# Kernel tuning notes

Measured on AMD Instinct MI355X. Metric: run time of the kernel, lower is better.

Reference implementation:

```python
import jax, jax.numpy as jnp
import numpy as np

EPS = 1e-6

def _rmsnorm(x, w):
    # Qwen3RMSNorm over last dim, computed in fp32
    var = jnp.mean(jnp.square(x), axis=-1, keepdims=True)
    return x * jax.lax.rsqrt(var + EPS) * w

def setup_inputs() -> dict:
    key = jax.random.key(0)
    ks = jax.random.split(key, 8)
    NSEQ, IN_DIM, H, G, D, SINK = 16384, 4096, 8, 4, 16, 16
    s = 0.02
    return {
        "hidden_states": jax.random.normal(ks[0], (1, NSEQ, IN_DIM), jnp.float32),
        "q_w": jax.random.normal(ks[1], (H * G * D, IN_DIM), jnp.float32) * s,
        "q_b": jax.random.normal(ks[2], (H * G * D,), jnp.float32) * s,
        "k_w": jax.random.normal(ks[3], (H * D, IN_DIM), jnp.float32) * s,
        "q_norm_w": jnp.ones((D,), jnp.float32),
        "k_norm_w": jnp.ones((D,), jnp.float32),
        "k_base": jax.random.normal(ks[4], (H, 1, SINK, D), jnp.float32) * s,
        "b": jax.random.normal(ks[5], (H, 1, G), jnp.float32) * s,
    }

def reference(hidden_states, q_w, q_b, k_w, q_norm_w, k_norm_w, k_base, b):
    H, _, SINK, D = k_base.shape
    G = b.shape[-1]
    d = jnp.sqrt(jnp.asarray(D, hidden_states.dtype))
    h = hidden_states[0]                                   # [n, in_dim]
    n = h.shape[0]
    # projections + RMSNorm
    q = _rmsnorm((h @ q_w.T + q_b).reshape(n, H, G, D), q_norm_w)   # [n,H,G,D]
    k = _rmsnorm((h @ k_w.T).reshape(n, H, D), k_norm_w)            # [n,H,D]
    # logit: per-token key against its own group queries + learned bias
    logit = jnp.einsum('nhd,nhgd->hng', k, q) / d + b               # [H,n,G]
    # logit_base: learned sink keys against queries
    logit_base = jnp.einsum('hsd,nhgd->hnsg', k_base[:, 0], q) / d  # [H,n,S,G]
    # sigmoid-difference gate, summed over sink tokens
    denom = 1.0 + jnp.sum(jnp.exp(logit_base - logit[:, :, None, :]), axis=2)  # [H,n,G]
    score = jnp.mean(1.0 / denom, axis=-1)                          # [H,n]
    return score[None]                                              # [1,H,n]
```

## Files before the change

kernel.cpp:

```cpp
#include <hip/hip_runtime.h>
#include <hip/hip_bf16.h>

typedef __attribute__((ext_vector_type(8))) short bf16x8;
typedef __attribute__((ext_vector_type(4))) float f32x4;
typedef unsigned short u16;

constexpr int NSEQ = 16384;
constexpr int KD   = 4096;
constexpr int NQ   = 512;
constexpr int NCOL = 640;
constexpr int BM   = 64;
constexpr int BK   = 32;
constexpr int KHALF = 2048;
constexpr int NKS  = KHALF / BK;
constexpr int WST_PER_KH = 64 * 8 * 5 * 64 * 8;
constexpr int WST_TT     = 8 * 5 * 64 * 8;
constexpr int WST_NB     = 5 * 64 * 8;
constexpr int WCONV_THREADS = 2 * 64 * 8 * 5 * 64;

__device__ __forceinline__ unsigned bf_round(float x) {
    unsigned u = __builtin_bit_cast(unsigned, x);
    unsigned r = u + 0x7FFFu + ((u >> 16) & 1u);
    return r >> 16;
}
__device__ __forceinline__ unsigned pk2(float lo, float hi) {
    return bf_round(lo) | (bf_round(hi) << 16);
}
__device__ __forceinline__ float bfu(unsigned u) {
    return __builtin_bit_cast(float, u << 16);
}

__global__ __launch_bounds__(256) void wconv_kernel(
    const float* __restrict__ qw, const float* __restrict__ kw,
    u16* __restrict__ Wst)
{
    int g = blockIdx.x * 256 + threadIdx.x;
    int lane = g & 63;
    int r  = g >> 6;
    int i  = r % 5;  r /= 5;
    int nblk = r & 7;  r >>= 3;
    int tt = r & 63;
    int kh = r >> 6;
    int n  = nblk * 80 + i * 16 + (lane & 15);
    int k0 = kh * KHALF + tt * BK + ((lane >> 4) << 3);
    const float* src = (n < NQ) ? (qw + (size_t)n * KD + k0)
                                : (kw + (size_t)(n - NQ) * KD + k0);
    float4 v0 = *(const float4*)(src);
    float4 v1 = *(const float4*)(src + 4);
    int4 o;
    o.x = (int)pk2(v0.x, v0.y);
    o.y = (int)pk2(v0.z, v0.w);
    o.z = (int)pk2(v1.x, v1.y);
    o.w = (int)pk2(v1.z, v1.w);
    *(int4*)(Wst + (size_t)g * 8) = o;
}

__global__ __launch_bounds__(512, 4) void gemm_kernel(
    const float* __restrict__ hid, const u16* __restrict__ Wst,
    u16* __restrict__ P0, u16* __restrict__ P1)
{
    __shared__ __align__(16) char smem[2 * 4096];

    const int t    = threadIdx.x;
    const int lane = t & 63;
    const int wid  = t >> 6;

    const int b    = blockIdx.x;
    const int xcd  = b & 7;
    const int kh   = xcd & 1;
    const int mblk = (b >> 3) * 4 + (xcd >> 1);
    const int row0 = mblk * BM;

    const float* hk = hid + (size_t)row0 * KD + kh * KHALF;
    const u16*   wb = Wst + (size_t)kh * WST_PER_KH + wid * WST_NB + lane * 8;
    u16* P = kh ? P1 : P0;

    f32x4 acc[4][5] = {};

    const int ar  = t >> 3;
    const int ks4 = t & 7;
    const float* gA = hk + (size_t)ar * KD + ks4 * 4;
    const int aWoff = ar * 64 + ((((ks4 >> 1) ^ ((ar >> 1) & 3)) << 4)
                                 + (ks4 & 1) * 8);

    const int bn   = lane & 15;
    const int koff = (((lane >> 4) ^ ((bn >> 1) & 3)) << 4);

    float4 s0, s1;

#define STEPX(TT, CUR, SW, SL, HG, HA)                                           \
    {                                                                            \
        const u16* wp = wb + (size_t)(TT) * WST_TT;                              \
        bf16x8 bf0 = *(const bf16x8*)(wp);                                       \
        bf16x8 bf1 = *(const bf16x8*)(wp + 512);                                 \
        bf16x8 bf2 = *(const bf16x8*)(wp + 1024);                                \
        bf16x8 bf3 = *(const bf16x8*)(wp + 1536);                                \
        bf16x8 bf4 = *(const bf16x8*)(wp + 2048);                                \
        if (HA) { SL = *(const float4*)(gA + ((TT) + 2) * BK); }                 \
        if (HG) {                                                                \
            int2 ap_;                                                            \
            ap_.x = (int)pk2(SW.x, SW.y);                                        \
            ap_.y = (int)pk2(SW.z, SW.w);                                        \
            *(int2*)(smem + ((CUR) ^ 1) * 4096 + aWoff) = ap_;                   \
        }                                                                        \
        const char* sAc = smem + (CUR) * 4096;                                   \
        _Pragma("unroll")                                                        \
        for (int m = 0; m < 4; ++m) {                                            \
            bf16x8 a_ = *(const bf16x8*)(sAc + (m * 16 + bn) * 64 + koff);       \
            acc[m][0] = __builtin_amdgcn_mfma_f32_16x16x32_bf16(a_, bf0, acc[m][0], 0, 0, 0); \
            acc[m][1] = __builtin_amdgcn_mfma_f32_16x16x32_bf16(a_, bf1, acc[m][1], 0, 0, 0); \
            acc[m][2] = __builtin_amdgcn_mfma_f32_16x16x32_bf16(a_, bf2, acc[m][2], 0, 0, 0); \
            acc[m][3] = __builtin_amdgcn_mfma_f32_16x16x32_bf16(a_, bf3, acc[m][3], 0, 0, 0); \
            acc[m][4] = __builtin_amdgcn_mfma_f32_16x16x32_bf16(a_, bf4, acc[m][4], 0, 0, 0); \
        }                                                                        \
        asm volatile("s_waitcnt lgkmcnt(0)" ::: "memory");                       \
        __builtin_amdgcn_s_barrier();                                            \
    }

    s0 = *(const float4*)(gA);
    s1 = *(const float4*)(gA + BK);
    {
        int2 ap_;
        ap_.x = (int)pk2(s0.x, s0.y);
        ap_.y = (int)pk2(s0.z, s0.w);
        *(int2*)(smem + aWoff) = ap_;
    }
    asm volatile("s_waitcnt lgkmcnt(0)" ::: "memory");
    __builtin_amdgcn_s_barrier();

#pragma unroll 1
    for (int t2 = 0; t2 < 31; ++t2) {
        const int tt = t2 * 2;
        STEPX(tt,     0, s1, s0, 1, 1)
        STEPX(tt + 1, 1, s0, s1, 1, 1)
    }
    STEPX(62, 0, s1, s0, 1, 0)
    STEPX(63, 1, s0, s1, 0, 0)
#undef STEPX

    const int crow = (lane >> 4) << 2;
    const int ccol = lane & 15;
    #pragma unroll
    for (int m = 0; m < 4; ++m)
        #pragma unroll
        for (int f = 0; f < 5; ++f)
            #pragma unroll
            for (int j = 0; j < 4; ++j)
                P[(size_t)(row0 + m * 16 + crow + j) * NCOL
                  + wid * 80 + f * 16 + ccol] = (u16)bf_round(acc[m][f][j]);
}

__global__ __launch_bounds__(256) void gate_kernel(
    const u16* __restrict__ P0, const u16* __restrict__ P1,
    const float* __restrict__ qb,
    const float* __restrict__ qnw, const float* __restrict__ knw,
    const float* __restrict__ kbase, const float* __restrict__ bb,
    float* __restrict__ out)
{
    __shared__ float skb[8 * 16 * 16];
    __shared__ float sqb[512];
    __shared__ float sb[32];
    __shared__ float snw[32];

    int tid = threadIdx.x;
    for (int i = tid; i < 2048; i += 256) skb[i] = kbase[i];
    for (int i = tid; i < 512;  i += 256) sqb[i] = qb[i];
    if (tid < 32) sb[tid] = bb[tid];
    if (tid < 16) snw[tid] = qnw[tid];
    else if (tid < 32) snw[tid] = knw[tid - 16];
    __syncthreads();

    int gid = blockIdx.x * 256 + tid;
    int tok = gid >> 5;
    int hh  = (gid >> 2) & 7;
    int g   = gid & 3;

    const u16* r0 = P0 + (size_t)tok * NCOL;
    const u16* r1 = P1 + (size_t)tok * NCOL;
    const int qoff = (hh * 4 + g) * 16;

    float q[16];
    float ss = 0.f;
    {
        int4 a0 = *(const int4*)(r0 + qoff);
        int4 a1 = *(const int4*)(r0 + qoff + 8);
        int4 b0 = *(const int4*)(r1 + qoff);
        int4 b1 = *(const int4*)(r1 + qoff + 8);
        int wa[8] = {a0.x, a0.y, a0.z, a0.w, a1.x, a1.y, a1.z, a1.w};
        int wb[8] = {b0.x, b0.y, b0.z, b0.w, b1.x, b1.y, b1.z, b1.w};
        #pragma unroll
        for (int i = 0; i < 8; ++i) {
            unsigned ua = (unsigned)wa[i], ub = (unsigned)wb[i];
            q[2*i+0] = bfu(ua & 0xFFFFu) + bfu(ub & 0xFFFFu) + sqb[qoff + 2*i+0];
            q[2*i+1] = bfu(ua >> 16)     + bfu(ub >> 16)     + sqb[qoff + 2*i+1];
        }
        #pragma unroll
        for (int d = 0; d < 16; ++d) ss += q[d] * q[d];
    }
    float rq = rsqrtf(ss * (1.f / 16.f) + 1e-6f);
    #pragma unroll
    for (int d = 0; d < 16; ++d) q[d] *= rq * snw[d];

    float k[16];
    float sk = 0.f;
    {
        const int koffb = NQ + hh * 16;
        int4 a0 = *(const int4*)(r0 + koffb);
        int4 a1 = *(const int4*)(r0 + koffb + 8);
        int4 b0 = *(const int4*)(r1 + koffb);
        int4 b1 = *(const int4*)(r1 + koffb + 8);
        int wa[8] = {a0.x, a0.y, a0.z, a0.w, a1.x, a1.y, a1.z, a1.w};
        int wb[8] = {b0.x, b0.y, b0.z, b0.w, b1.x, b1.y, b1.z, b1.w};
        #pragma unroll
        for (int i = 0; i < 8; ++i) {
            unsigned ua = (unsigned)wa[i], ub = (unsigned)wb[i];
            k[2*i+0] = bfu(ua & 0xFFFFu) + bfu(ub & 0xFFFFu);
            k[2*i+1] = bfu(ua >> 16)     + bfu(ub >> 16);
        }
        #pragma unroll
        for (int d = 0; d < 16; ++d) sk += k[d] * k[d];
    }
    float rk = rsqrtf(sk * (1.f / 16.f) + 1e-6f);

    float logit = 0.f;
    #pragma unroll
    for (int d = 0; d < 16; ++d) logit += (k[d] * rk * snw[16 + d]) * q[d];
    logit = logit * 0.25f + sb[hh * 4 + g];

    float accum = 0.f;
    const float* kbh = skb + hh * 256;
    #pragma unroll
    for (int s = 0; s < 16; ++s) {
        float lb = 0.f;
        #pragma unroll
        for (int d = 0; d < 16; ++d) lb += kbh[s * 16 + d] * q[d];
        accum += __expf(lb * 0.25f - logit);
    }
    float r = 1.f / (1.f + accum);

    r += __shfl_xor(r, 1);
    r += __shfl_xor(r, 2);
    if (g == 0) out[(size_t)hh * NSEQ + tok] = r * 0.25f;
}

extern "C" void kernel_launch(void* const* d_in, const int* in_sizes, int n_in,
                              void* d_out, int out_size, void* d_ws, size_t ws_size,
                              hipStream_t stream)
{
    const float* hid = (const float*)d_in[0];
    const float* qw  = (const float*)d_in[1];
    const float* qb  = (const float*)d_in[2];
    const float* kw  = (const float*)d_in[3];
    const float* qnw = (const float*)d_in[4];
    const float* knw = (const float*)d_in[5];
    const float* kb  = (const float*)d_in[6];
    const float* bb  = (const float*)d_in[7];
    float* out = (float*)d_out;

    u16* Wst = (u16*)d_ws;
    u16* P0  = (u16*)((char*)d_ws + (size_t)NCOL * KD * 2);
    u16* P1  = P0 + (size_t)NSEQ * NCOL;

    wconv_kernel<<<WCONV_THREADS / 256, 256, 0, stream>>>(qw, kw, Wst);
    gemm_kernel<<<512, 512, 0, stream>>>(hid, Wst, P0, P1);
    gate_kernel<<<NSEQ * 32 / 256, 256, 0, stream>>>(P0, P1, qb, qnw, knw, kb, bb, out);
}
```

Baseline: 158.7 us.

## Load A fragments directly from global memory, dropping LDS staging and barriers

The GEMM kernel stops staging the fp32 hidden-state tile through double-buffered shared memory with a barrier every k-step. Each wave now loads its own A fragments straight from global memory, converts them to bf16 in registers, and feeds them to the MFMAs. The min-blocks-per-CU launch bound is also dropped. This removes LDS traffic and block-wide synchronisation, but all 8 waves now each fetch the same A rows (8x redundant global/L2 reads of a large fp32 matrix) and lose the explicit software prefetch, so the loop may become memory-latency bound.

```diff
diff --git a/kernel.cpp b/kernel.cpp
--- a/kernel.cpp
+++ b/kernel.cpp
@@ -55,12 +55,10 @@
     *(int4*)(Wst + (size_t)g * 8) = o;
 }
 
-__global__ __launch_bounds__(512, 4) void gemm_kernel(
+__global__ __launch_bounds__(512) void gemm_kernel(
     const float* __restrict__ hid, const u16* __restrict__ Wst,
     u16* __restrict__ P0, u16* __restrict__ P1)
 {
-    __shared__ __align__(16) char smem[2 * 4096];
-
     const int t    = threadIdx.x;
     const int lane = t & 63;
     const int wid  = t >> 6;
@@ -71,72 +69,56 @@
     const int mblk = (b >> 3) * 4 + (xcd >> 1);
     const int row0 = mblk * BM;
 
-    const float* hk = hid + (size_t)row0 * KD + kh * KHALF;
-    const u16*   wb = Wst + (size_t)kh * WST_PER_KH + wid * WST_NB + lane * 8;
+    const u16* wb = Wst + (size_t)kh * WST_PER_KH + wid * WST_NB + lane * 8;
     u16* P = kh ? P1 : P0;
 
+    const int bn = lane & 15;
+    const int ks = lane >> 4;
+
+    const float* aP0 = hid + (size_t)(row0 +  0 + bn) * KD + kh * KHALF + ks * 8;
+    const float* aP1 = hid + (size_t)(row0 + 16 + bn) * KD + kh * KHALF + ks * 8;
+    const float* aP2 = hid + (size_t)(row0 + 32 + bn) * KD + kh * KHALF + ks * 8;
+    const float* aP3 = hid + (size_t)(row0 + 48 + bn) * KD + kh * KHALF + ks * 8;
+
     f32x4 acc[4][5] = {};
 
-    const int ar  = t >> 3;
-    const int ks4 = t & 7;
-    const float* gA = hk + (size_t)ar * KD + ks4 * 4;
-    const int aWoff = ar * 64 + ((((ks4 >> 1) ^ ((ar >> 1) & 3)) << 4)
-                                 + (ks4 & 1) * 8);
-
-    const int bn   = lane & 15;
-    const int koff = (((lane >> 4) ^ ((bn >> 1) & 3)) << 4);
-
-    float4 s0, s1;
-
-#define STEPX(TT, CUR, SW, SL, HG, HA)                                           \
+#define AFRAG(PTR, OUT)                                                          \
     {                                                                            \
-        const u16* wp = wb + (size_t)(TT) * WST_TT;                              \
-        bf16x8 bf0 = *(const bf16x8*)(wp);                                       \
-        bf16x8 bf1 = *(const bf16x8*)(wp + 512);                                 \
-        bf16x8 bf2 = *(const bf16x8*)(wp + 1024);                                \
-        bf16x8 bf3 = *(const bf16x8*)(wp + 1536);                                \
-        bf16x8 bf4 = *(const bf16x8*)(wp + 2048);                                \
-        if (HA) { SL = *(const float4*)(gA + ((TT) + 2) * BK); }                 \
-        if (HG) {                                                                \
-            int2 ap_;                                                            \
-            ap_.x = (int)pk2(SW.x, SW.y);                                        \
-            ap_.y = (int)pk2(SW.z, SW.w);                                        \
-            *(int2*)(smem + ((CUR) ^ 1) * 4096 + aWoff) = ap_;                   \
-        }                                                                        \
-        const char* sAc = smem + (CUR) * 4096;                                   \
-        _Pragma("unroll")                                                        \
-        for (int m = 0; m < 4; ++m) {                                            \
-            bf16x8 a_ = *(const bf16x8*)(sAc + (m * 16 + bn) * 64 + koff);       \
-            acc[m][0] = __builtin_amdgcn_mfma_f32_16x16x32_bf16(a_, bf0, acc[m][0], 0, 0, 0); \
-            acc[m][1] = __builtin_amdgcn_mfma_f32_16x16x32_bf16(a_, bf1, acc[m][1], 0, 0, 0); \
-            acc[m][2] = __builtin_amdgcn_mfma_f32_16x16x32_bf16(a_, bf2, acc[m][2], 0, 0, 0); \
-            acc[m][3] = __builtin_amdgcn_mfma_f32_16x16x32_bf16(a_, bf3, acc[m][3], 0, 0, 0); \
-            acc[m][4] = __builtin_amdgcn_mfma_f32_16x16x32_bf16(a_, bf4, acc[m][4], 0, 0, 0); \
-        }                                                                        \
-        asm volatile("s_waitcnt lgkmcnt(0)" ::: "memory");                       \
-        __builtin_amdgcn_s_barrier();                                            \
-    }
-
-    s0 = *(const float4*)(gA);
-    s1 = *(const float4*)(gA + BK);
-    {
-        int2 ap_;
-        ap_.x = (int)pk2(s0.x, s0.y);
-        ap_.y = (int)pk2(s0.z, s0.w);
-        *(int2*)(smem + aWoff) = ap_;
-    }
-    asm volatile("s_waitcnt lgkmcnt(0)" ::: "memory");
-    __builtin_amdgcn_s_barrier();
-
-#pragma unroll 1
-    for (int t2 = 0; t2 < 31; ++t2) {
-        const int tt = t2 * 2;
-        STEPX(tt,     0, s1, s0, 1, 1)
-        STEPX(tt + 1, 1, s0, s1, 1, 1)
-    }
-    STEPX(62, 0, s1, s0, 1, 0)
-    STEPX(63, 1, s0, s1, 0, 0)
-#undef STEPX
+        float4 va_ = *(const float4*)((PTR) + (size_t)tt * BK);                  \
+        float4 vb_ = *(const float4*)((PTR) + (size_t)tt * BK + 4);              \
+        int4 w_;                                                                 \
+        w_.x = (int)pk2(va_.x, va_.y);  w_.y = (int)pk2(va_.z, va_.w);           \
+        w_.z = (int)pk2(vb_.x, vb_.y);  w_.w = (int)pk2(vb_.z, vb_.w);           \
+        OUT = __builtin_bit_cast(bf16x8, w_);                                    \
+    }
+
+#define MROW(AF, M)                                                              \
+    acc[M][0] = __builtin_amdgcn_mfma_f32_16x16x32_bf16(AF, f0, acc[M][0], 0, 0, 0); \
+    acc[M][1] = __builtin_amdgcn_mfma_f32_16x16x32_bf16(AF, f1, acc[M][1], 0, 0, 0); \
+    acc[M][2] = __builtin_amdgcn_mfma_f32_16x16x32_bf16(AF, f2, acc[M][2], 0, 0, 0); \
+    acc[M][3] = __builtin_amdgcn_mfma_f32_16x16x32_bf16(AF, f3, acc[M][3], 0, 0, 0); \
+    acc[M][4] = __builtin_amdgcn_mfma_f32_16x16x32_bf16(AF, f4, acc[M][4], 0, 0, 0)
+
+#pragma unroll 2
+    for (int tt = 0; tt < NKS; ++tt) {
+        const u16* wp = wb + (size_t)tt * WST_TT;
+        bf16x8 f0 = *(const bf16x8*)(wp);
+        bf16x8 f1 = *(const bf16x8*)(wp + 512);
+        bf16x8 f2 = *(const bf16x8*)(wp + 1024);
+        bf16x8 f3 = *(const bf16x8*)(wp + 1536);
+        bf16x8 f4 = *(const bf16x8*)(wp + 2048);
+        bf16x8 a0f, a1f, a2f, a3f;
+        AFRAG(aP0, a0f)
+        AFRAG(aP1, a1f)
+        AFRAG(aP2, a2f)
+        AFRAG(aP3, a3f)
+        MROW(a0f, 0);
+        MROW(a1f, 1);
+        MROW(a2f, 2);
+        MROW(a3f, 3);
+    }
+#undef AFRAG
+#undef MROW
 
     const int crow = (lane >> 4) << 2;
     const int ccol = lane & 15;
```

Measured after the change: 437.5 us. +175.6%, slower.
